# Performance work log

Measured on AMD Instinct MI355X. Metric: run time of the kernel, lower is better.

Reference implementation:

```python
import jax, jax.numpy as jnp
import numpy as np

N, FIN, H, FOUT = 4096, 128, 4, 64
NEG_INF = -1e9


def _xavier(key, shape):
    fan_in, fan_out = shape[-2], shape[-1]
    limit = float(np.sqrt(6.0 / (fan_in + fan_out)))
    return jax.random.uniform(key, shape, jnp.float32, -limit, limit)


def setup_inputs() -> dict:
    key = jax.random.key(0)
    ks = jax.random.split(key, 7)
    x = jax.random.normal(ks[0], (N, FIN), jnp.float32)
    u = jax.random.uniform(ks[1], (N, N))
    mask = jnp.where(u < 0.02, 0.0, NEG_INF).astype(jnp.float32)
    idx = jnp.arange(N)
    mask = mask.at[idx, idx].set(0.0)
    proj_param = _xavier(ks[2], (H, FIN, FOUT))          # per-head projection
    score_src = _xavier(ks[3], (H, FOUT, 1))             # scoring_fn_source (IMP1 layout)
    score_tgt = _xavier(ks[4], (H, FOUT, 1))             # scoring_fn_target
    skip_w = _xavier(ks[5], (H * FOUT, FIN))             # skip_proj Linear weight
    bias = jnp.zeros((H * FOUT,), jnp.float32)
    return {"x": x, "mask": mask, "proj_param": proj_param,
            "score_src": score_src, "score_tgt": score_tgt,
            "skip_w": skip_w, "bias": bias}


def reference(x, mask, proj_param, score_src, score_tgt, skip_w, bias):
    # project: [1,N,Fin] @ [H,Fin,Fout] -> [H,N,Fout]
    h = jnp.einsum('nf,hfo->hno', x, proj_param)
    # additive (Bahdanau-style) scores
    s_src = jnp.matmul(h, score_src)                     # [H,N,1]
    s_tgt = jnp.matmul(h, score_tgt)                     # [H,N,1]
    all_scores = jax.nn.leaky_relu(s_src + jnp.swapaxes(s_tgt, 1, 2), 0.2)  # [H,N,N]
    attn = jax.nn.softmax(all_scores + mask[None, :, :], axis=-1)           # [H,N,N]
    # aggregate: [H,N,N] @ [H,N,Fout] -> [N,H,Fout]
    out = jnp.einsum('hnm,hmo->nho', attn, h)
    # skip connection (dims differ: Fin != H*Fout -> use skip_proj)
    out = out + jnp.matmul(x, skip_w.T).reshape(N, H, FOUT)
    out = out.reshape(N, H * FOUT) + bias                # concat heads + bias
    return jax.nn.elu(out)
```

## Files before the change

kernel.cpp:

```cpp
#include <hip/hip_runtime.h>
#include <hip/hip_bf16.h>
#include <math.h>


#define NN   4096
#define FIN  128
#define NH   4
#define FO   64
#define HF   256
#define SEG  96

typedef unsigned short ushort_t;
typedef unsigned int uint4n __attribute__((ext_vector_type(4)));

__device__ __forceinline__ ushort_t f2bf(float f) {
    __hip_bfloat16 h = __float2bfloat16(f);
    union { __hip_bfloat16 h; ushort_t u; } c; c.h = h; return c.u;
}
__device__ __forceinline__ float bf2f(ushort_t u) {
    union { unsigned int i; float f; } c; c.i = ((unsigned int)u) << 16; return c.f;
}

__global__ __launch_bounds__(256) void k1_gemm(
        const float* __restrict__ x,
        const float* __restrict__ proj,
        const float* __restrict__ skw,
        const float* __restrict__ asrc,
        const float* __restrict__ atgt,
        ushort_t* __restrict__ h2b, float* __restrict__ skip_ws,
        float* __restrict__ src4, float* __restrict__ tgt4) {
    __shared__ float sA[64 * 132];
    __shared__ float sB[128 * 64];
    const int tid = threadIdx.x;
    const int bc  = blockIdx.x;
    const int i0  = blockIdx.y * 64;

    {
        const float4* src = (const float4*)(x + (size_t)i0 * FIN);
        #pragma unroll
        for (int q = 0; q < 8; q++) {
            int s   = tid + q * 256;
            int row = s >> 5;
            int c4  = (s & 31) << 2;
            float4 v = src[s];
            float* d = sA + row * 132 + c4;
            d[0] = v.x; d[1] = v.y; d[2] = v.z; d[3] = v.w;
        }
    }
    if (bc < 4) {
        const float4* src = (const float4*)(proj + (size_t)bc * FIN * FO);
        #pragma unroll
        for (int q = 0; q < 8; q++) {
            int s = tid + q * 256;
            *(float4*)(sB + (size_t)s * 4) = src[s];
        }
    } else {
        const float* sw = skw + (size_t)(bc - 4) * 64 * FIN;
        #pragma unroll
        for (int q = 0; q < 8; q++) {
            int s  = tid + q * 256;
            int c  = s & 63;
            int k4 = (s >> 6) << 2;
            float4 v = *(const float4*)(sw + (size_t)c * FIN + k4);
            sB[(k4 + 0) * 64 + c] = v.x;
            sB[(k4 + 1) * 64 + c] = v.y;
            sB[(k4 + 2) * 64 + c] = v.z;
            sB[(k4 + 3) * 64 + c] = v.w;
        }
    }
    __syncthreads();

    const int tx = tid & 15, ty = tid >> 4;
    const int r0 = ty << 2, c0 = tx << 2;
    float acc[4][4] = {};
    #pragma unroll 2
    for (int k = 0; k < FIN; k += 4) {
        alignas(16) float a[4][4];
        alignas(16) float b[4][4];
        #pragma unroll
        for (int rr = 0; rr < 4; rr++)
            *(float4*)a[rr] = *(const float4*)(sA + (r0 + rr) * 132 + k);
        #pragma unroll
        for (int kk = 0; kk < 4; kk++)
            *(float4*)b[kk] = *(const float4*)(sB + (k + kk) * 64 + c0);
        #pragma unroll
        for (int kk = 0; kk < 4; kk++)
            #pragma unroll
            for (int rr = 0; rr < 4; rr++)
                #pragma unroll
                for (int cc = 0; cc < 4; cc++)
                    acc[rr][cc] = fmaf(a[rr][kk], b[kk][cc], acc[rr][cc]);
    }

    if (bc < 4) {
        #pragma unroll
        for (int rr = 0; rr < 4; rr++) {
            ushort4 hv;
            hv.x = f2bf(acc[rr][0]); hv.y = f2bf(acc[rr][1]);
            hv.z = f2bf(acc[rr][2]); hv.w = f2bf(acc[rr][3]);
            *(ushort4*)(h2b + (size_t)(i0 + r0 + rr) * HF + bc * 64 + c0) = hv;
        }
        float as[4], at[4];
        #pragma unroll
        for (int cc = 0; cc < 4; cc++) {
            as[cc] = asrc[bc * FO + c0 + cc];
            at[cc] = atgt[bc * FO + c0 + cc];
        }
        #pragma unroll
        for (int rr = 0; rr < 4; rr++) {
            float ps = acc[rr][0] * as[0] + acc[rr][1] * as[1]
                     + acc[rr][2] * as[2] + acc[rr][3] * as[3];
            float pt = acc[rr][0] * at[0] + acc[rr][1] * at[1]
                     + acc[rr][2] * at[2] + acc[rr][3] * at[3];
            #pragma unroll
            for (int off = 8; off >= 1; off >>= 1) {
                ps += __shfl_xor(ps, off, 64);
                pt += __shfl_xor(pt, off, 64);
            }
            if (tx == 0) {
                int i = i0 + r0 + rr;
                src4[(size_t)i * 4 + bc] = ps;
                tgt4[(size_t)i * 4 + bc] = pt;
            }
        }
    } else {
        float* dst = skip_ws + (size_t)i0 * HF + (bc - 4) * 64;
        #pragma unroll
        for (int rr = 0; rr < 4; rr++)
            *(float4*)(dst + (size_t)(r0 + rr) * HF + c0) = *(float4*)acc[rr];
    }
}

__global__ __launch_bounds__(256) void k2_attn(
        const unsigned int* __restrict__ mask,
        const ushort_t* __restrict__ h2b,
        const float* __restrict__ skip_ws,
        const float* __restrict__ src4,
        const float* __restrict__ tgt4,
        const float* __restrict__ bias,
        float* __restrict__ out) {
    __shared__ int   s_nbr[4 * SEG];
    __shared__ float s_p[4][4 * SEG];
    __shared__ int   s_ct[4];
    const int tid  = threadIdx.x;
    const int lane = tid & 63, w = tid >> 6;
    const int i    = blockIdx.x;
    const int col  = w * 64 + lane;

    const float skipv = skip_ws[(size_t)i * HF + col];
    const float bv    = bias[col];
    const float sc    = src4[(size_t)i * 4 + w];

    const uint4n* mrow = (const uint4n*)(mask + (size_t)i * NN);
    uint4n mv[4];
    #pragma unroll
    for (int s = 0; s < 4; s++)
        mv[s] = __builtin_nontemporal_load(&mrow[w * 256 + s * 64 + lane]);

    int base = 0;
    #pragma unroll
    for (int s = 0; s < 4; s++) {
        #pragma unroll
        for (int e = 0; e < 4; e++) {
            bool hit = (mv[s][e] & 0x7fffffffu) == 0u;
            unsigned long long bal = __ballot(hit);
            int pre = __builtin_amdgcn_mbcnt_hi(
                          (unsigned int)(bal >> 32),
                          __builtin_amdgcn_mbcnt_lo((unsigned int)bal, 0));
            if (hit) {
                int slot = base + pre;
                if (slot < SEG)
                    s_nbr[w * SEG + slot] = w * 1024 + s * 256 + lane * 4 + e;
            }
            base += (int)__popcll(bal);
        }
    }
    if (lane == 0) s_ct[w] = base < SEG ? base : SEG;
    __syncthreads();

    int cts[4];
    #pragma unroll
    for (int s = 0; s < 4; s++) cts[s] = s_ct[s];
    float lsum = 0.f;
    #pragma unroll
    for (int s = 0; s < 4; s++) {
        for (int kk = lane; kk < cts[s]; kk += 64) {
            int j = s_nbr[s * SEG + kk];
            float p = sc + tgt4[(size_t)j * 4 + w];
            p = p > 0.f ? p : 0.2f * p;
            p = __expf(p);
            s_p[w][s * SEG + kk] = p;
            lsum += p;
        }
    }
    #pragma unroll
    for (int off = 32; off >= 1; off >>= 1)
        lsum += __shfl_xor(lsum, off, 64);
    const float inv = lsum > 0.f ? 1.0f / lsum : 0.0f;

    const ushort_t* hp = h2b + col;
    const float* pp = s_p[w];
    float acc = 0.f;
    #pragma unroll
    for (int s = 0; s < 4; s++) {
        const int ct = cts[s];
        const int* nb = s_nbr + s * SEG;
        const float* ps = pp + s * SEG;
        int kk = 0;
        for (; kk + 8 <= ct; kk += 8) {
            int j0 = nb[kk + 0], j1 = nb[kk + 1], j2 = nb[kk + 2], j3 = nb[kk + 3];
            int j4 = nb[kk + 4], j5 = nb[kk + 5], j6 = nb[kk + 6], j7 = nb[kk + 7];
            float p0 = ps[kk + 0], p1 = ps[kk + 1], p2 = ps[kk + 2], p3 = ps[kk + 3];
            float p4 = ps[kk + 4], p5 = ps[kk + 5], p6 = ps[kk + 6], p7 = ps[kk + 7];
            float h0 = bf2f(hp[(size_t)j0 * HF]);
            float h1 = bf2f(hp[(size_t)j1 * HF]);
            float h2v = bf2f(hp[(size_t)j2 * HF]);
            float h3 = bf2f(hp[(size_t)j3 * HF]);
            float h4 = bf2f(hp[(size_t)j4 * HF]);
            float h5 = bf2f(hp[(size_t)j5 * HF]);
            float h6 = bf2f(hp[(size_t)j6 * HF]);
            float h7 = bf2f(hp[(size_t)j7 * HF]);
            acc = fmaf(p0, h0, acc);  acc = fmaf(p1, h1, acc);
            acc = fmaf(p2, h2v, acc); acc = fmaf(p3, h3, acc);
            acc = fmaf(p4, h4, acc);  acc = fmaf(p5, h5, acc);
            acc = fmaf(p6, h6, acc);  acc = fmaf(p7, h7, acc);
        }
        for (; kk < ct; kk++)
            acc = fmaf(ps[kk], bf2f(hp[(size_t)nb[kk] * HF]), acc);
    }

    float vv = acc * inv + skipv + bv;
    vv = vv > 0.f ? vv : expm1f(vv);
    out[(size_t)i * HF + col] = vv;
}

extern "C" void kernel_launch(void* const* d_in, const int* in_sizes, int n_in,
                              void* d_out, int out_size, void* d_ws, size_t ws_size,
                              hipStream_t stream) {
    const float*        x    = (const float*)d_in[0];
    const unsigned int* mask = (const unsigned int*)d_in[1];
    const float*        proj = (const float*)d_in[2];
    const float*        asrc = (const float*)d_in[3];
    const float*        atgt = (const float*)d_in[4];
    const float*        skw  = (const float*)d_in[5];
    const float*        bias = (const float*)d_in[6];
    float*              out  = (float*)d_out;

    char* ws = (char*)d_ws;
    ushort_t* h2b     = (ushort_t*)ws;
    float*    skip_ws = (float*)(ws + (2u << 20));
    float*    src4    = (float*)(ws + (6u << 20));
    float*    tgt4    = (float*)(ws + (6u << 20) + (64u << 10));

    hipLaunchKernelGGL(k1_gemm, dim3(8, 64), dim3(256), 0, stream,
                       x, proj, skw, asrc, atgt, h2b, skip_ws, src4, tgt4);
    hipLaunchKernelGGL(k2_attn, dim3(4096), dim3(256), 0, stream,
                       mask, h2b, skip_ws, src4, tgt4, bias, out);
}
```

Measured before the change: 143.8 us.

## Split mask scan into separate kernel emitting compacted neighbor lists

The fused attention kernel is split in two. A new scan kernel reads the dense mask and writes a per-row list of 16-bit neighbor indices plus a count to workspace. It runs before the projection GEMM on the same stream. The attention kernel then loads the short list into shared memory and runs a single flattened gather loop instead of four per-segment loops, which removes the mask streaming and ballot work from the gather kernel. In exchange there is an extra launch, a small global write and read of the lists, and a total cap of 192 neighbors per row in addition to the existing 96-per-quarter cap.

New measurement: 144.6 us. No clear change (+0.6%).

```diff
diff --git a/kernel.cpp b/kernel.cpp
--- a/kernel.cpp
+++ b/kernel.cpp
@@ -9,6 +9,7 @@
 #define FO   64
 #define HF   256
 #define SEG  96
+#define LIST 192
 
 typedef unsigned short ushort_t;
 typedef unsigned int uint4n __attribute__((ext_vector_type(4)));
@@ -131,25 +132,15 @@
     }
 }
 
-__global__ __launch_bounds__(256) void k2_attn(
+__global__ __launch_bounds__(256) void k2a_scan(
         const unsigned int* __restrict__ mask,
-        const ushort_t* __restrict__ h2b,
-        const float* __restrict__ skip_ws,
-        const float* __restrict__ src4,
-        const float* __restrict__ tgt4,
-        const float* __restrict__ bias,
-        float* __restrict__ out) {
-    __shared__ int   s_nbr[4 * SEG];
-    __shared__ float s_p[4][4 * SEG];
-    __shared__ int   s_ct[4];
+        ushort_t* __restrict__ list,
+        int* __restrict__ cnt) {
+    __shared__ ushort_t s_nbr[4 * SEG];
+    __shared__ int s_wt[4];
     const int tid  = threadIdx.x;
     const int lane = tid & 63, w = tid >> 6;
     const int i    = blockIdx.x;
-    const int col  = w * 64 + lane;
-
-    const float skipv = skip_ws[(size_t)i * HF + col];
-    const float bv    = bias[col];
-    const float sc    = src4[(size_t)i * 4 + w];
 
     const uint4n* mrow = (const uint4n*)(mask + (size_t)i * NN);
     uint4n mv[4];
@@ -170,28 +161,63 @@
             if (hit) {
                 int slot = base + pre;
                 if (slot < SEG)
-                    s_nbr[w * SEG + slot] = w * 1024 + s * 256 + lane * 4 + e;
+                    s_nbr[w * SEG + slot] =
+                        (ushort_t)(w * 1024 + s * 256 + lane * 4 + e);
             }
             base += (int)__popcll(bal);
         }
     }
-    if (lane == 0) s_ct[w] = base < SEG ? base : SEG;
+    if (lane == 0) s_wt[w] = base < SEG ? base : SEG;
     __syncthreads();
 
-    int cts[4];
-    #pragma unroll
-    for (int s = 0; s < 4; s++) cts[s] = s_ct[s];
+    const int t0 = s_wt[0], t1 = s_wt[1], t2 = s_wt[2], t3 = s_wt[3];
+    const int off = (w > 0 ? t0 : 0) + (w > 1 ? t1 : 0) + (w > 2 ? t2 : 0);
+    const int mine = s_wt[w];
+    ushort_t* dst = list + (size_t)i * LIST;
+    for (int kk = lane; kk < mine; kk += 64) {
+        int p = off + kk;
+        if (p < LIST) dst[p] = s_nbr[w * SEG + kk];
+    }
+    if (tid == 0) {
+        int tot = t0 + t1 + t2 + t3;
+        cnt[i] = tot < LIST ? tot : LIST;
+    }
+}
+
+__global__ __launch_bounds__(256) void k2b_attn(
+        const ushort_t* __restrict__ list,
+        const int* __restrict__ cnt,
+        const ushort_t* __restrict__ h2b,
+        const float* __restrict__ skip_ws,
+        const float* __restrict__ src4,
+        const float* __restrict__ tgt4,
+        const float* __restrict__ bias,
+        float* __restrict__ out) {
+    __shared__ float s_p[4][LIST];
+    __shared__ int   s_j[LIST];
+    const int tid  = threadIdx.x;
+    const int lane = tid & 63, w = tid >> 6;
+    const int i    = blockIdx.x;
+    const int col  = w * 64 + lane;
+
+    const float skipv = skip_ws[(size_t)i * HF + col];
+    const float bv    = bias[col];
+    const float sc    = src4[(size_t)i * 4 + w];
+    int c = cnt[i];
+    c = c < LIST ? c : LIST;
+
+    const ushort_t* lp = list + (size_t)i * LIST;
+    for (int kk = tid; kk < c; kk += 256) s_j[kk] = lp[kk];
+    __syncthreads();
+
     float lsum = 0.f;
-    #pragma unroll
-    for (int s = 0; s < 4; s++) {
-        for (int kk = lane; kk < cts[s]; kk += 64) {
-            int j = s_nbr[s * SEG + kk];
-            float p = sc + tgt4[(size_t)j * 4 + w];
-            p = p > 0.f ? p : 0.2f * p;
-            p = __expf(p);
-            s_p[w][s * SEG + kk] = p;
-            lsum += p;
-        }
+    for (int kk = lane; kk < c; kk += 64) {
+        int j = s_j[kk];
+        float p = sc + tgt4[(size_t)j * 4 + w];
+        p = p > 0.f ? p : 0.2f * p;
+        p = __expf(p);
+        s_p[w][kk] = p;
+        lsum += p;
     }
     #pragma unroll
     for (int off = 32; off >= 1; off >>= 1)
@@ -199,35 +225,29 @@
     const float inv = lsum > 0.f ? 1.0f / lsum : 0.0f;
 
     const ushort_t* hp = h2b + col;
-    const float* pp = s_p[w];
+    const float* ps = s_p[w];
     float acc = 0.f;
-    #pragma unroll
-    for (int s = 0; s < 4; s++) {
-        const int ct = cts[s];
-        const int* nb = s_nbr + s * SEG;
-        const float* ps = pp + s * SEG;
-        int kk = 0;
-        for (; kk + 8 <= ct; kk += 8) {
-            int j0 = nb[kk + 0], j1 = nb[kk + 1], j2 = nb[kk + 2], j3 = nb[kk + 3];
-            int j4 = nb[kk + 4], j5 = nb[kk + 5], j6 = nb[kk + 6], j7 = nb[kk + 7];
-            float p0 = ps[kk + 0], p1 = ps[kk + 1], p2 = ps[kk + 2], p3 = ps[kk + 3];
-            float p4 = ps[kk + 4], p5 = ps[kk + 5], p6 = ps[kk + 6], p7 = ps[kk + 7];
-            float h0 = bf2f(hp[(size_t)j0 * HF]);
-            float h1 = bf2f(hp[(size_t)j1 * HF]);
-            float h2v = bf2f(hp[(size_t)j2 * HF]);
-            float h3 = bf2f(hp[(size_t)j3 * HF]);
-            float h4 = bf2f(hp[(size_t)j4 * HF]);
-            float h5 = bf2f(hp[(size_t)j5 * HF]);
-            float h6 = bf2f(hp[(size_t)j6 * HF]);
-            float h7 = bf2f(hp[(size_t)j7 * HF]);
-            acc = fmaf(p0, h0, acc);  acc = fmaf(p1, h1, acc);
-            acc = fmaf(p2, h2v, acc); acc = fmaf(p3, h3, acc);
-            acc = fmaf(p4, h4, acc);  acc = fmaf(p5, h5, acc);
-            acc = fmaf(p6, h6, acc);  acc = fmaf(p7, h7, acc);
-        }
-        for (; kk < ct; kk++)
-            acc = fmaf(ps[kk], bf2f(hp[(size_t)nb[kk] * HF]), acc);
-    }
+    int kk = 0;
+    for (; kk + 8 <= c; kk += 8) {
+        int j0 = s_j[kk + 0], j1 = s_j[kk + 1], j2 = s_j[kk + 2], j3 = s_j[kk + 3];
+        int j4 = s_j[kk + 4], j5 = s_j[kk + 5], j6 = s_j[kk + 6], j7 = s_j[kk + 7];
+        float p0 = ps[kk + 0], p1 = ps[kk + 1], p2 = ps[kk + 2], p3 = ps[kk + 3];
+        float p4 = ps[kk + 4], p5 = ps[kk + 5], p6 = ps[kk + 6], p7 = ps[kk + 7];
+        float h0 = bf2f(hp[(size_t)j0 * HF]);
+        float h1 = bf2f(hp[(size_t)j1 * HF]);
+        float h2v = bf2f(hp[(size_t)j2 * HF]);
+        float h3 = bf2f(hp[(size_t)j3 * HF]);
+        float h4 = bf2f(hp[(size_t)j4 * HF]);
+        float h5 = bf2f(hp[(size_t)j5 * HF]);
+        float h6 = bf2f(hp[(size_t)j6 * HF]);
+        float h7 = bf2f(hp[(size_t)j7 * HF]);
+        acc = fmaf(p0, h0, acc);  acc = fmaf(p1, h1, acc);
+        acc = fmaf(p2, h2v, acc); acc = fmaf(p3, h3, acc);
+        acc = fmaf(p4, h4, acc);  acc = fmaf(p5, h5, acc);
+        acc = fmaf(p6, h6, acc);  acc = fmaf(p7, h7, acc);
+    }
+    for (; kk < c; kk++)
+        acc = fmaf(ps[kk], bf2f(hp[(size_t)s_j[kk] * HF]), acc);
 
     float vv = acc * inv + skipv + bv;
     vv = vv > 0.f ? vv : expm1f(vv);
@@ -251,9 +271,13 @@
     float*    skip_ws = (float*)(ws + (2u << 20));
     float*    src4    = (float*)(ws + (6u << 20));
     float*    tgt4    = (float*)(ws + (6u << 20) + (64u << 10));
-
+    ushort_t* list    = (ushort_t*)(ws + (8u << 20));
+    int*      cntp    = (int*)(ws + (10u << 20));
+
+    hipLaunchKernelGGL(k2a_scan, dim3(4096), dim3(256), 0, stream,
+                       mask, list, cntp);
     hipLaunchKernelGGL(k1_gemm, dim3(8, 64), dim3(256), 0, stream,
                        x, proj, skw, asrc, atgt, h2b, skip_ws, src4, tgt4);
-    hipLaunchKernelGGL(k2_attn, dim3(4096), dim3(256), 0, stream,
-                       mask, h2b, skip_ws, src4, tgt4, bias, out);
-}
+    hipLaunchKernelGGL(k2b_attn, dim3(4096), dim3(256), 0, stream,
+                       list, cntp, h2b, skip_ws, src4, tgt4, bias, out);
+}
```
